# Performance work log

Measured on AMD Instinct MI355X. Metric: run time of the kernel, lower is better.

Reference implementation:

```python
import jax, jax.numpy as jnp
import numpy as np

D_K = 766  # feature dim, also softmax temperature per module init
NEG = -1000000000.0


def setup_inputs() -> dict:
    key = jax.random.key(0)
    k1, k2, k3 = jax.random.split(key, 3)
    B, H, L, D = 2, 4, 2048, D_K
    Q = jax.random.normal(k1, (B, H, L, D), dtype=jnp.float32)
    K = jax.random.normal(k2, (B, H, L, D), dtype=jnp.float32)
    attn_mask = jax.random.randint(k3, (B, H, L, L), 0, 2) > 0  # bool [B,H,Lk,Lq]
    return {"Q": Q, "K": K, "attn_mask": attn_mask}


def reference(Q, K, attn_mask):
    # scores: [B,H,Lq,Lk]
    scores = jnp.einsum("bhqd,bhkd->bhqk", Q, K) / np.sqrt(D_K).astype(np.float32)
    # mask is [B,H,Lk,Lq]; torch applies mask.transpose(2,3)
    scores = jnp.where(jnp.swapaxes(attn_mask, 2, 3), NEG, scores)
    attn1 = jax.nn.softmax(scores, axis=-1)                       # row softmax
    attn2 = jax.nn.softmax(jnp.swapaxes(scores, -1, -2), axis=-1)  # col softmax
    # dropout prob = 0.0 -> identity
    context1 = jnp.einsum("bhqk,bhkd->bhqd", attn1, K)
    context2 = jnp.einsum("bhkq,bhqd->bhkd", attn2, Q)
    return (context1, context2, attn1, attn2)
```

## Files before the change

### kernel.cpp

```cpp
#include <hip/hip_runtime.h>
#include <math.h>

#define L 2048
#define DK 766
#define DKP 768
#define NBH 8
#define NR (NBH * L)
#define NEGV -1000000000.0f

typedef __attribute__((ext_vector_type(8))) short bf16x8_t;
typedef __attribute__((ext_vector_type(4))) float f32x4_t;

#define LDT 72

typedef __attribute__((address_space(1))) const unsigned int gu32;
typedef __attribute__((address_space(3))) unsigned int lu32;

__device__ __forceinline__ short f2bf(float x) {
    union { float f; unsigned u; } v;
    v.f = x;
    unsigned r = v.u + 0x7fff + ((v.u >> 16) & 1);
    return (short)(r >> 16);
}

__device__ __forceinline__ float bf2f(short s) {
    union { unsigned u; float f; } v;
    v.u = ((unsigned)(unsigned short)s) << 16;
    return v.f;
}

__device__ __forceinline__ void gl_lds16(const void* g, void* l) {
    __builtin_amdgcn_global_load_lds((gu32*)g, (lu32*)l, 16, 0, 0);
}

#define BARR() asm volatile("s_barrier" ::: "memory")
#define VMW() asm volatile("s_waitcnt vmcnt(0)" ::: "memory")
#define PRIO1() __builtin_amdgcn_s_setprio(1)
#define PRIO0() __builtin_amdgcn_s_setprio(0)

__global__ __launch_bounds__(256) void k_cvtT(const float* __restrict__ Q,
                                              const float* __restrict__ K,
                                              short* __restrict__ Qb,
                                              short* __restrict__ Kb,
                                              short* __restrict__ Qt,
                                              short* __restrict__ Kt) {
    __shared__ short T[64 * LDT];
    const int tz = blockIdx.z;
    const int bh = tz & 7;
    const float* X = (tz < 8) ? Q : K;
    short* Xb = (tz < 8) ? Qb : Kb;
    short* Xt = (tz < 8) ? Qt : Kt;
    X += (size_t)bh * L * DK;
    Xb += (size_t)bh * L * DKP;
    Xt += (size_t)bh * DKP * L;
    const int r0 = blockIdx.y * 64, c0 = blockIdx.x * 64;
    const int t = threadIdx.x;
    const int rl = t >> 2, cc = (t & 3) * 16;

    bf16x8_t v0, v1;
#pragma unroll
    for (int p = 0; p < 8; ++p) {
        int c = c0 + cc + 2 * p;
        float2 f = (c < DK) ? *(const float2*)&X[(size_t)(r0 + rl) * DK + c]
                            : make_float2(0.f, 0.f);
        if (p < 4) { v0[2 * p] = f2bf(f.x); v0[2 * p + 1] = f2bf(f.y); }
        else { v1[2 * (p - 4)] = f2bf(f.x); v1[2 * (p - 4) + 1] = f2bf(f.y); }
    }
    *(bf16x8_t*)&Xb[(size_t)(r0 + rl) * DKP + c0 + cc] = v0;
    *(bf16x8_t*)&Xb[(size_t)(r0 + rl) * DKP + c0 + cc + 8] = v1;
    *(bf16x8_t*)&T[rl * LDT + cc] = v0;
    *(bf16x8_t*)&T[rl * LDT + cc + 8] = v1;
    __syncthreads();
    bf16x8_t w0, w1;
#pragma unroll
    for (int p = 0; p < 8; ++p) {
        w0[p] = T[(cc + p) * LDT + rl];
        w1[p] = T[(cc + 8 + p) * LDT + rl];
    }
    *(bf16x8_t*)&Xt[(size_t)(c0 + rl) * L + r0 + cc] = w0;
    *(bf16x8_t*)&Xt[(size_t)(c0 + rl) * L + r0 + cc + 8] = w1;
}

__global__ __launch_bounds__(512, 2) void k_score8(const short* __restrict__ Kb,
                                                   const short* __restrict__ Qb,
                                                   const int* __restrict__ mask,
                                                   short* __restrict__ Sb,
                                                   float* __restrict__ prowM,
                                                   float* __restrict__ prowS,
                                                   float* __restrict__ pcolM,
                                                   float* __restrict__ pcolS) {
    __shared__ __align__(16) short LB[65536];

    int flat = blockIdx.x;
    int nw = (flat & 7) * 64 + (flat >> 3);
    int bh = nw >> 6, rem = nw & 63;
    int byp = rem >> 3, bxp = rem & 7;
    const short* Am = Kb + (size_t)bh * L * DKP;
    const short* Bm = Qb + (size_t)bh * L * DKP;
    const int* Mm = mask + (size_t)bh * L * L;
    short* Sm = Sb + (size_t)bh * L * L;
    const int m0 = byp * 256, n0 = bxp * 256;

    const int t = threadIdx.x, lane = t & 63, wid = t >> 6;
    const int wr = wid >> 2, wc = wid & 3;
    const int lr = lane & 15, lg = lane >> 4;

    const int schunk = (lane & 7) ^ (lane >> 3);
    const short* aSrc = Am + (size_t)(m0 + wid * 8 + (lane >> 3)) * DKP + schunk * 8;
    const short* bSrc = Bm + (size_t)(n0 + wid * 8 + (lane >> 3)) * DKP + schunk * 8;
    char* ldsA = (char*)LB;
    char* ldsB = (char*)LB + 65536;

#define STAGEA(cb, k0n)                                                                 \
    do {                                                                                \
        gl_lds16(aSrc + (k0n), ldsA + (cb)*32768 + wid * 1024);                         \
        gl_lds16(aSrc + (size_t)64 * DKP + (k0n), ldsA + (cb)*32768 + 8192 + wid * 1024);  \
        gl_lds16(aSrc + (size_t)128 * DKP + (k0n), ldsA + (cb)*32768 + 16384 + wid * 1024); \
        gl_lds16(aSrc + (size_t)192 * DKP + (k0n), ldsA + (cb)*32768 + 24576 + wid * 1024); \
    } while (0)
#define STAGEB(cb, k0n)                                                                 \
    do {                                                                                \
        gl_lds16(bSrc + (k0n), ldsB + (cb)*32768 + wid * 1024);                         \
        gl_lds16(bSrc + (size_t)64 * DKP + (k0n), ldsB + (cb)*32768 + 8192 + wid * 1024);  \
        gl_lds16(bSrc + (size_t)128 * DKP + (k0n), ldsB + (cb)*32768 + 16384 + wid * 1024); \
        gl_lds16(bSrc + (size_t)192 * DKP + (k0n), ldsB + (cb)*32768 + 24576 + wid * 1024); \
    } while (0)

    const int axr = lr & 7;
    const int kc0 = ((0 + lg) ^ axr) * 8;
    const int kc1 = ((4 + lg) ^ axr) * 8;
    const int aRd = wr * 8192 + lr * 64;
    const int bRd = 32768 + (wc >> 1) * 8192 + ((wc & 1) * 64 + lr) * 64;

#define LDA0(c, i) (*(const bf16x8_t*)&LB[(c)*16384 + aRd + (i)*1024 + kc0])
#define LDA1(c, i) (*(const bf16x8_t*)&LB[(c)*16384 + aRd + (i)*1024 + kc1])
#define LDB0(c, j) (*(const bf16x8_t*)&LB[(c)*16384 + bRd + (j)*1024 + kc0])
#define LDB1(c, j) (*(const bf16x8_t*)&LB[(c)*16384 + bRd + (j)*1024 + kc1])

    f32x4_t acc[8][4];
#pragma unroll
    for (int i = 0; i < 8; ++i)
#pragma unroll
        for (int j = 0; j < 4; ++j) acc[i][j] = f32x4_t{0.f, 0.f, 0.f, 0.f};

    bf16x8_t bfr[4][2];

#define PHASE(c, i0, EXTRA)                                                             \
    do {                                                                                \
        bf16x8_t a00 = LDA0(c, i0), a01 = LDA1(c, i0);                                  \
        bf16x8_t a10 = LDA0(c, (i0) + 1), a11 = LDA1(c, (i0) + 1);                      \
        EXTRA;                                                                          \
        BARR();                                                                         \
        PRIO1();                                                                        \
        _Pragma("unroll") for (int j = 0; j < 4; ++j) {                                 \
            acc[i0][j] = __builtin_amdgcn_mfma_f32_16x16x32_bf16(a00, bfr[j][0],        \
                                                                 acc[i0][j], 0, 0, 0);  \
            acc[i0][j] = __builtin_amdgcn_mfma_f32_16x16x32_bf16(a01, bfr[j][1],        \
                                                                 acc[i0][j], 0, 0, 0);  \
            acc[(i0) + 1][j] = __builtin_amdgcn_mfma_f32_16x16x32_bf16(                 \
                a10, bfr[j][0], acc[(i0) + 1][j], 0, 0, 0);                             \
            acc[(i0) + 1][j] = __builtin_amdgcn_mfma_f32_16x16x32_bf16(                 \
                a11, bfr[j][1], acc[(i0) + 1][j], 0, 0, 0);                             \
        }                                                                               \
        PRIO0();                                                                        \
    } while (0)

    const int NT = DKP / 64;
    STAGEA(0, 0);
    STAGEB(0, 0);
    VMW();
    BARR();

    for (int kt = 0; kt < NT; ++kt) {
        const int c = kt & 1;
        const bool ds = (kt + 1 < NT);
        const int k0n = (kt + 1) * 64;
#pragma unroll
        for (int j = 0; j < 4; ++j) {
            bfr[j][0] = LDB0(c, j);
            bfr[j][1] = LDB1(c, j);
        }
        PHASE(c, 0, if (ds) STAGEA(c ^ 1, k0n));
        BARR();
        PHASE(c, 2, if (ds) STAGEB(c ^ 1, k0n));
        BARR();
        PHASE(c, 4, ((void)0));
        BARR();
        PHASE(c, 6, ((void)0));
        if (ds) VMW();
        BARR();
    }

    const float scale = 1.0f / sqrtf((float)DK);
#pragma unroll
    for (int i = 0; i < 8; ++i) {
        int krow = m0 + wr * 128 + i * 16 + lg * 4;
#pragma unroll
        for (int j = 0; j < 4; ++j) {
            int qcol = n0 + wc * 64 + j * 16 + lr;
#pragma unroll
            for (int r = 0; r < 4; ++r) {
                int mv = Mm[(size_t)(krow + r) * L + qcol];
                float v = mv ? NEGV : acc[i][j][r] * scale;
                acc[i][j][r] = v;
                Sm[(size_t)(krow + r) * L + qcol] = f2bf(v);
            }
        }
    }

    __syncthreads();
    float* redb = (float*)LB;

#pragma unroll
    for (int i = 0; i < 8; ++i) {
#pragma unroll
        for (int r = 0; r < 4; ++r) {
            float rm = fmaxf(fmaxf(acc[i][0][r], acc[i][1][r]),
                             fmaxf(acc[i][2][r], acc[i][3][r]));
#pragma unroll
            for (int m = 1; m < 16; m <<= 1) rm = fmaxf(rm, __shfl_xor(rm, m, 64));
            float rs = 0.f;
#pragma unroll
            for (int j = 0; j < 4; ++j) rs += expf(acc[i][j][r] - rm);
#pragma unroll
            for (int m = 1; m < 16; m <<= 1) rs += __shfl_xor(rs, m, 64);
            if (lr == 0) {
                int kr = wr * 128 + i * 16 + lg * 4 + r;
                redb[wc * 256 + kr] = rm;
                redb[1024 + wc * 256 + kr] = rs;
            }
        }
    }
#pragma unroll
    for (int j = 0; j < 4; ++j) {
        float cm = -INFINITY;
#pragma unroll
        for (int i = 0; i < 8; ++i)
#pragma unroll
            for (int r = 0; r < 4; ++r) cm = fmaxf(cm, acc[i][j][r]);
        cm = fmaxf(cm, __shfl_xor(cm, 16, 64));
        cm = fmaxf(cm, __shfl_xor(cm, 32, 64));
        float cs = 0.f;
#pragma unroll
        for (int i = 0; i < 8; ++i)
#pragma unroll
            for (int r = 0; r < 4; ++r) cs += expf(acc[i][j][r] - cm);
        cs += __shfl_xor(cs, 16, 64);
        cs += __shfl_xor(cs, 32, 64);
        if (lg == 0) {
            int qc = wc * 64 + j * 16 + lr;
            redb[2048 + wr * 256 + qc] = cm;
            redb[2560 + wr * 256 + qc] = cs;
        }
    }
    __syncthreads();
    if (t < 256) {
        float m = redb[t];
        float s = 0.f;
#pragma unroll
        for (int w = 1; w < 4; ++w) m = fmaxf(m, redb[w * 256 + t]);
#pragma unroll
        for (int w = 0; w < 4; ++w)
            s += redb[1024 + w * 256 + t] * expf(redb[w * 256 + t] - m);
        size_t o = (size_t)bxp * NR + bh * L + m0 + t;
        prowM[o] = m;
        prowS[o] = s;
    } else {
        int qc = t - 256;
        float mA = redb[2048 + qc], mB = redb[2048 + 256 + qc];
        float sA = redb[2560 + qc], sB = redb[2560 + 256 + qc];
        float m = fmaxf(mA, mB);
        float s = sA * expf(mA - m) + sB * expf(mB - m);
        size_t o = (size_t)byp * NR + bh * L + n0 + qc;
        pcolM[o] = m;
        pcolS[o] = s;
    }
#undef PHASE
#undef STAGEA
#undef STAGEB
#undef LDA0
#undef LDA1
#undef LDB0
#undef LDB1
}

__global__ __launch_bounds__(256) void k_comb8(const float* __restrict__ prowM,
                                               const float* __restrict__ prowS,
                                               const float* __restrict__ pcolM,
                                               const float* __restrict__ pcolS,
                                               float* __restrict__ m1,
                                               float* __restrict__ r1,
                                               float* __restrict__ m2,
                                               float* __restrict__ r2) {
    int idx = blockIdx.x * 256 + threadIdx.x;
    float m = -INFINITY;
#pragma unroll
    for (int c = 0; c < 8; ++c) m = fmaxf(m, prowM[(size_t)c * NR + idx]);
    float s = 0.f;
#pragma unroll
    for (int c = 0; c < 8; ++c)
        s += prowS[(size_t)c * NR + idx] * expf(prowM[(size_t)c * NR + idx] - m);
    m2[idx] = m;
    r2[idx] = 1.0f / s;

    m = -INFINITY;
#pragma unroll
    for (int c = 0; c < 8; ++c) m = fmaxf(m, pcolM[(size_t)c * NR + idx]);
    s = 0.f;
#pragma unroll
    for (int c = 0; c < 8; ++c)
        s += pcolS[(size_t)c * NR + idx] * expf(pcolM[(size_t)c * NR + idx] - m);
    m1[idx] = m;
    r1[idx] = 1.0f / s;
}

__global__ __launch_bounds__(256) void k_apply(const short* __restrict__ Sb,
                                               const float* __restrict__ mr,
                                               const float* __restrict__ rr,
                                               const float* __restrict__ mc,
                                               const float* __restrict__ rc,
                                               float* __restrict__ OutIn,
                                               float* __restrict__ OutTr,
                                               short* __restrict__ bIn,
                                               short* __restrict__ bTr) {
    __shared__ float T[64][65];
    const int bh = blockIdx.z;
    const int rb0 = blockIdx.x * 64, cb0 = blockIdx.y * 64;
    const short* Sm = Sb + (size_t)bh * L * L;
    float* Oin = OutIn + (size_t)bh * L * L;
    float* Otr = OutTr + (size_t)bh * L * L;
    const int t = threadIdx.x, tx = t & 15, ty = t >> 4;

    float4 mcv = *(const float4*)&mc[bh * L + cb0 + tx * 4];
    float4 rcv = *(const float4*)&rc[bh * L + cb0 + tx * 4];

#pragma unroll
    for (int i = 0; i < 4; ++i) {
        int r = rb0 + ty * 4 + i;
        float mrv = mr[bh * L + r], rrv = rr[bh * L + r];
        short4 sx = *(const short4*)&Sm[(size_t)r * L + cb0 + tx * 4];
        float x0 = bf2f(sx.x), x1 = bf2f(sx.y), x2 = bf2f(sx.z), x3 = bf2f(sx.w);
        float4 e = make_float4(expf(x0 - mrv) * rrv, expf(x1 - mrv) * rrv,
                               expf(x2 - mrv) * rrv, expf(x3 - mrv) * rrv);
        *(float4*)&Oin[(size_t)r * L + cb0 + tx * 4] = e;
        short4 b = make_short4(f2bf(e.x), f2bf(e.y), f2bf(e.z), f2bf(e.w));
        *(short4*)&bIn[(size_t)bh * L * L + (size_t)r * L + cb0 + tx * 4] = b;
        T[tx * 4 + 0][ty * 4 + i] = expf(x0 - mcv.x) * rcv.x;
        T[tx * 4 + 1][ty * 4 + i] = expf(x1 - mcv.y) * rcv.y;
        T[tx * 4 + 2][ty * 4 + i] = expf(x2 - mcv.z) * rcv.z;
        T[tx * 4 + 3][ty * 4 + i] = expf(x3 - mcv.w) * rcv.w;
    }
    __syncthreads();
#pragma unroll
    for (int i = 0; i < 4; ++i) {
        int c = ty * 4 + i;
        float4 v = make_float4(T[c][tx * 4], T[c][tx * 4 + 1], T[c][tx * 4 + 2],
                               T[c][tx * 4 + 3]);
        *(float4*)&Otr[(size_t)(cb0 + c) * L + rb0 + tx * 4] = v;
        short4 b = make_short4(f2bf(v.x), f2bf(v.y), f2bf(v.z), f2bf(v.w));
        *(short4*)&bTr[(size_t)bh * L * L + (size_t)(cb0 + c) * L + rb0 + tx * 4] = b;
    }
}

__global__ __launch_bounds__(512, 2) void k_ctx8(const short* __restrict__ a1b,
                                                 const short* __restrict__ a2b,
                                                 const short* __restrict__ Kt,
                                                 const short* __restrict__ Qt,
                                                 float* __restrict__ c1,
                                                 float* __restrict__ c2) {
    __shared__ __align__(16) short LB[57344];

    int flat = blockIdx.x;
    int nw = (flat & 7) * 64 + (flat >> 3);
    int inst = nw >> 5, rem = nw & 31;
    int myp = rem >> 2, nxp = rem & 3;
    int bh = inst & 7;
    const short* Am = ((inst < 8) ? a1b : a2b) + (size_t)bh * L * L;
    const short* Bt = ((inst < 8) ? Kt : Qt) + (size_t)bh * DKP * L;
    float* Cm = ((inst < 8) ? c1 : c2) + (size_t)bh * L * DK;
    const int m0 = myp * 256, n0 = nxp * 192;

    const int t = threadIdx.x, lane = t & 63, wid = t >> 6;
    const int wr = wid >> 2, wc = wid & 3;
    const int lr = lane & 15, lg = lane >> 4;

    const int schunk = (lane & 7) ^ (lane >> 3);
    const short* aSrc = Am + (size_t)(m0 + wid * 8 + (lane >> 3)) * L + schunk * 8;
    const short* bSrc = Bt + (size_t)(n0 + wid * 8 + (lane >> 3)) * L + schunk * 8;
    char* ldsA = (char*)LB;
    char* ldsB = (char*)LB + 65536;

#define STAGEA(cb, k0n)                                                               \
    do {                                                                              \
        gl_lds16(aSrc + (k0n), ldsA + (cb)*32768 + wid * 1024);                       \
        gl_lds16(aSrc + (size_t)64 * L + (k0n), ldsA + (cb)*32768 + 8192 + wid * 1024); \
        gl_lds16(aSrc + (size_t)128 * L + (k0n), ldsA + (cb)*32768 + 16384 + wid * 1024); \
        gl_lds16(aSrc + (size_t)192 * L + (k0n), ldsA + (cb)*32768 + 24576 + wid * 1024); \
    } while (0)
#define STAGEB(cb, k0n)                                                               \
    do {                                                                              \
        gl_lds16(bSrc + (k0n), ldsB + (cb)*24576 + wid * 1024);                       \
        gl_lds16(bSrc + (size_t)64 * L + (k0n), ldsB + (cb)*24576 + 8192 + wid * 1024); \
        gl_lds16(bSrc + (size_t)128 * L + (k0n), ldsB + (cb)*24576 + 16384 + wid * 1024); \
    } while (0)

    const int axr = lr & 7;
    const int kc0 = ((0 + lg) ^ axr) * 8;
    const int kc1 = ((4 + lg) ^ axr) * 8;
    const int aRd = wr * 8192 + lr * 64;
    const int bRd = 32768 + (wc * 48 + lr) * 64;

#define LDA0(c, i) (*(const bf16x8_t*)&LB[(c)*16384 + aRd + (i)*1024 + kc0])
#define LDA1(c, i) (*(const bf16x8_t*)&LB[(c)*16384 + aRd + (i)*1024 + kc1])
#define LDB0(c, j) (*(const bf16x8_t*)&LB[bRd + (c)*12288 + (j)*1024 + kc0])
#define LDB1(c, j) (*(const bf16x8_t*)&LB[bRd + (c)*12288 + (j)*1024 + kc1])

    f32x4_t acc[8][3];
#pragma unroll
    for (int i = 0; i < 8; ++i)
#pragma unroll
        for (int j = 0; j < 3; ++j) acc[i][j] = f32x4_t{0.f, 0.f, 0.f, 0.f};

    bf16x8_t bfr[3][2];

#define PHASE(c, i0, EXTRA)                                                           \
    do {                                                                              \
        bf16x8_t a00 = LDA0(c, i0), a01 = LDA1(c, i0);                                \
        bf16x8_t a10 = LDA0(c, (i0) + 1), a11 = LDA1(c, (i0) + 1);                    \
        EXTRA;                                                                        \
        BARR();                                                                       \
        PRIO1();                                                                      \
        _Pragma("unroll") for (int j = 0; j < 3; ++j) {                               \
            acc[i0][j] = __builtin_amdgcn_mfma_f32_16x16x32_bf16(a00, bfr[j][0],      \
                                                                 acc[i0][j], 0, 0, 0); \
            acc[i0][j] = __builtin_amdgcn_mfma_f32_16x16x32_bf16(a01, bfr[j][1],      \
                                                                 acc[i0][j], 0, 0, 0); \
            acc[(i0) + 1][j] = __builtin_amdgcn_mfma_f32_16x16x32_bf16(               \
                a10, bfr[j][0], acc[(i0) + 1][j], 0, 0, 0);                           \
            acc[(i0) + 1][j] = __builtin_amdgcn_mfma_f32_16x16x32_bf16(               \
                a11, bfr[j][1], acc[(i0) + 1][j], 0, 0, 0);                           \
        }                                                                             \
        PRIO0();                                                                      \
    } while (0)

    const int NT = L / 64;
    STAGEA(0, 0);
    STAGEB(0, 0);
    VMW();
    BARR();

    for (int kt = 0; kt < NT; ++kt) {
        const int c = kt & 1;
        const bool ds = (kt + 1 < NT);
        const int k0n = (kt + 1) * 64;
#pragma unroll
        for (int j = 0; j < 3; ++j) {
            bfr[j][0] = LDB0(c, j);
            bfr[j][1] = LDB1(c, j);
        }
        PHASE(c, 0, if (ds) STAGEA(c ^ 1, k0n));
        BARR();
        PHASE(c, 2, if (ds) STAGEB(c ^ 1, k0n));
        BARR();
        PHASE(c, 4, ((void)0));
        BARR();
        PHASE(c, 6, ((void)0));
        if (ds) VMW();
        BARR();
    }

#pragma unroll
    for (int i = 0; i < 8; ++i) {
        int row = m0 + wr * 128 + i * 16 + lg * 4;
#pragma unroll
        for (int j = 0; j < 3; ++j) {
            int col = n0 + wc * 48 + j * 16 + lr;
            if (col < DK) {
#pragma unroll
                for (int r = 0; r < 4; ++r)
                    Cm[(size_t)(row + r) * DK + col] = acc[i][j][r];
            }
        }
    }
#undef PHASE
#undef STAGEA
#undef STAGEB
#undef LDA0
#undef LDA1
#undef LDB0
#undef LDB1
}

extern "C" void kernel_launch(void* const* d_in, const int* in_sizes, int n_in,
                              void* d_out, int out_size, void* d_ws, size_t ws_size,
                              hipStream_t stream) {
    const float* Q = (const float*)d_in[0];
    const float* K = (const float*)d_in[1];
    const int* mask = (const int*)d_in[2];
    float* out = (float*)d_out;

    const size_t CTX = (size_t)NBH * L * DK;
    const size_t ATT = (size_t)NBH * L * L;
    float* c1 = out;
    float* c2 = out + CTX;
    float* a1 = out + 2 * CTX;
    float* a2 = out + 2 * CTX + ATT;

    float* ws = (float*)d_ws;
    float* m1 = ws;
    float* r1 = ws + NR;
    float* m2 = ws + 2 * (size_t)NR;
    float* r2 = ws + 3 * (size_t)NR;
    const size_t QBE = (size_t)NBH * L * DKP;
    short* Qb = (short*)(ws + 4 * (size_t)NR);
    short* Kb = Qb + QBE;
    short* a1b = Kb + QBE;
    short* a2b = a1b + ATT;
    short* Qt = a2b + ATT;
    short* Kt = Qt + QBE;

    float* prowM = c1;
    float* prowS = c1 + 8 * (size_t)NR;
    float* pcolM = c1 + 16 * (size_t)NR;
    float* pcolS = c1 + 24 * (size_t)NR;

    dim3 blk(256);

    k_cvtT<<<dim3(12, 32, 16), blk, 0, stream>>>(Q, K, Qb, Kb, Qt, Kt);
    k_score8<<<dim3(512), dim3(512), 0, stream>>>(Kb, Qb, mask, a2b, prowM, prowS,
                                                  pcolM, pcolS);
    k_comb8<<<dim3(NR / 256), blk, 0, stream>>>(prowM, prowS, pcolM, pcolS, m1, r1,
                                                m2, r2);
    k_apply<<<dim3(32, 32, NBH), blk, 0, stream>>>(a2b, m2, r2, m1, r1, a2, a1, a2b,
                                                   a1b);
    k_ctx8<<<dim3(512), dim3(512), 0, stream>>>(a1b, a2b, Kt, Qt, c1, c2);
}
```

Baseline: 431.8 us.

## Make score blocks compute two adjacent output tiles with prefetch across tiles

Each k_score8 workgroup now processes two 256x256 score tiles sharing the same K rows, halving the grid to 256 blocks. The first k-chunk of the second tile's operands is prefetched during the last k-step of the first tile, so the epilogue (mask, store, softmax partials) of tile one overlaps with loads for tile two. The reduction buffer moves to a different LDS region to avoid clobbering the prefetched data. This cuts per-block startup and pipeline-fill cost, but gives fewer blocks than CUs (256 on a 256-CU part at 2 blocks/CU occupancy), which may leave some parallelism unused.

```diff
diff --git a/kernel.cpp b/kernel.cpp
--- a/kernel.cpp
+++ b/kernel.cpp
@@ -92,14 +92,14 @@
     __shared__ __align__(16) short LB[65536];
 
     int flat = blockIdx.x;
-    int nw = (flat & 7) * 64 + (flat >> 3);
-    int bh = nw >> 6, rem = nw & 63;
-    int byp = rem >> 3, bxp = rem & 7;
+    int nw = (flat & 7) * 32 + (flat >> 3);
+    int bh = nw >> 5, rem = nw & 31;
+    int byp = rem >> 2, bxq = rem & 3;
     const short* Am = Kb + (size_t)bh * L * DKP;
     const short* Bm = Qb + (size_t)bh * L * DKP;
     const int* Mm = mask + (size_t)bh * L * L;
     short* Sm = Sb + (size_t)bh * L * L;
-    const int m0 = byp * 256, n0 = bxp * 256;
+    const int m0 = byp * 256;
 
     const int t = threadIdx.x, lane = t & 63, wid = t >> 6;
     const int wr = wid >> 2, wc = wid & 3;
@@ -107,23 +107,24 @@
 
     const int schunk = (lane & 7) ^ (lane >> 3);
     const short* aSrc = Am + (size_t)(m0 + wid * 8 + (lane >> 3)) * DKP + schunk * 8;
-    const short* bSrc = Bm + (size_t)(n0 + wid * 8 + (lane >> 3)) * DKP + schunk * 8;
+    const short* bSrc0 =
+        Bm + (size_t)(bxq * 512 + wid * 8 + (lane >> 3)) * DKP + schunk * 8;
     char* ldsA = (char*)LB;
     char* ldsB = (char*)LB + 65536;
 
-#define STAGEA(cb, k0n)                                                                 \
+#define STAGEAp(P, cb, k0n)                                                             \
     do {                                                                                \
-        gl_lds16(aSrc + (k0n), ldsA + (cb)*32768 + wid * 1024);                         \
-        gl_lds16(aSrc + (size_t)64 * DKP + (k0n), ldsA + (cb)*32768 + 8192 + wid * 1024);  \
-        gl_lds16(aSrc + (size_t)128 * DKP + (k0n), ldsA + (cb)*32768 + 16384 + wid * 1024); \
-        gl_lds16(aSrc + (size_t)192 * DKP + (k0n), ldsA + (cb)*32768 + 24576 + wid * 1024); \
+        gl_lds16((P) + (k0n), ldsA + (cb)*32768 + wid * 1024);                          \
+        gl_lds16((P) + (size_t)64 * DKP + (k0n), ldsA + (cb)*32768 + 8192 + wid * 1024);   \
+        gl_lds16((P) + (size_t)128 * DKP + (k0n), ldsA + (cb)*32768 + 16384 + wid * 1024); \
+        gl_lds16((P) + (size_t)192 * DKP + (k0n), ldsA + (cb)*32768 + 24576 + wid * 1024); \
     } while (0)
-#define STAGEB(cb, k0n)                                                                 \
+#define STAGEBp(P, cb, k0n)                                                             \
     do {                                                                                \
-        gl_lds16(bSrc + (k0n), ldsB + (cb)*32768 + wid * 1024);                         \
-        gl_lds16(bSrc + (size_t)64 * DKP + (k0n), ldsB + (cb)*32768 + 8192 + wid * 1024);  \
-        gl_lds16(bSrc + (size_t)128 * DKP + (k0n), ldsB + (cb)*32768 + 16384 + wid * 1024); \
-        gl_lds16(bSrc + (size_t)192 * DKP + (k0n), ldsB + (cb)*32768 + 24576 + wid * 1024); \
+        gl_lds16((P) + (k0n), ldsB + (cb)*32768 + wid * 1024);                          \
+        gl_lds16((P) + (size_t)64 * DKP + (k0n), ldsB + (cb)*32768 + 8192 + wid * 1024);   \
+        gl_lds16((P) + (size_t)128 * DKP + (k0n), ldsB + (cb)*32768 + 16384 + wid * 1024); \
+        gl_lds16((P) + (size_t)192 * DKP + (k0n), ldsB + (cb)*32768 + 24576 + wid * 1024); \
     } while (0)
 
     const int axr = lr & 7;
@@ -138,11 +139,6 @@
 #define LDB1(c, j) (*(const bf16x8_t*)&LB[(c)*16384 + bRd + (j)*1024 + kc1])
 
     f32x4_t acc[8][4];
-#pragma unroll
-    for (int i = 0; i < 8; ++i)
-#pragma unroll
-        for (int j = 0; j < 4; ++j) acc[i][j] = f32x4_t{0.f, 0.f, 0.f, 0.f};
-
     bf16x8_t bfr[4][2];
 
 #define PHASE(c, i0, EXTRA)                                                             \
@@ -166,118 +162,148 @@
     } while (0)
 
     const int NT = DKP / 64;
-    STAGEA(0, 0);
-    STAGEB(0, 0);
-    VMW();
-    BARR();
-
-    for (int kt = 0; kt < NT; ++kt) {
-        const int c = kt & 1;
-        const bool ds = (kt + 1 < NT);
-        const int k0n = (kt + 1) * 64;
+
+    for (int pp = 0; pp < 2; ++pp) {
+        const int bxp = bxq * 2 + pp;
+        const int n0 = bxp * 256;
+        const short* bSrc = bSrc0 + (size_t)pp * 256 * DKP;
+        const short* bSrcN = bSrc0 + (size_t)256 * DKP;
+
+#pragma unroll
+        for (int i = 0; i < 8; ++i)
+#pragma unroll
+            for (int j = 0; j < 4; ++j) acc[i][j] = f32x4_t{0.f, 0.f, 0.f, 0.f};
+
+        if (pp == 0) {
+            STAGEAp(aSrc, 0, 0);
+            STAGEBp(bSrc, 0, 0);
+        }
+        VMW();
+        BARR();
+
+        for (int kt = 0; kt < NT - 1; ++kt) {
+            const int c = kt & 1;
+            const int k0n = (kt + 1) * 64;
+#pragma unroll
+            for (int j = 0; j < 4; ++j) {
+                bfr[j][0] = LDB0(c, j);
+                bfr[j][1] = LDB1(c, j);
+            }
+            PHASE(c, 0, STAGEAp(aSrc, c ^ 1, k0n));
+            BARR();
+            PHASE(c, 2, STAGEBp(bSrc, c ^ 1, k0n));
+            BARR();
+            PHASE(c, 4, ((void)0));
+            BARR();
+            PHASE(c, 6, ((void)0));
+            VMW();
+            BARR();
+        }
+        {
+            const int c = 1;
+#pragma unroll
+            for (int j = 0; j < 4; ++j) {
+                bfr[j][0] = LDB0(c, j);
+                bfr[j][1] = LDB1(c, j);
+            }
+            PHASE(c, 0, if (pp == 0) STAGEAp(aSrc, 0, 0));
+            BARR();
+            PHASE(c, 2, if (pp == 0) STAGEBp(bSrcN, 0, 0));
+            BARR();
+            PHASE(c, 4, ((void)0));
+            BARR();
+            PHASE(c, 6, ((void)0));
+            BARR();
+        }
+
+        const float scale = 1.0f / sqrtf((float)DK);
+#pragma unroll
+        for (int i = 0; i < 8; ++i) {
+            int krow = m0 + wr * 128 + i * 16 + lg * 4;
+#pragma unroll
+            for (int j = 0; j < 4; ++j) {
+                int qcol = n0 + wc * 64 + j * 16 + lr;
+#pragma unroll
+                for (int r = 0; r < 4; ++r) {
+                    int mv = Mm[(size_t)(krow + r) * L + qcol];
+                    float v = mv ? NEGV : acc[i][j][r] * scale;
+                    acc[i][j][r] = v;
+                    Sm[(size_t)(krow + r) * L + qcol] = f2bf(v);
+                }
+            }
+        }
+
+        __syncthreads();
+        float* redb = (float*)&LB[16384];
+
+#pragma unroll
+        for (int i = 0; i < 8; ++i) {
+#pragma unroll
+            for (int r = 0; r < 4; ++r) {
+                float rm = fmaxf(fmaxf(acc[i][0][r], acc[i][1][r]),
+                                 fmaxf(acc[i][2][r], acc[i][3][r]));
+#pragma unroll
+                for (int m = 1; m < 16; m <<= 1) rm = fmaxf(rm, __shfl_xor(rm, m, 64));
+                float rs = 0.f;
+#pragma unroll
+                for (int j = 0; j < 4; ++j) rs += expf(acc[i][j][r] - rm);
+#pragma unroll
+                for (int m = 1; m < 16; m <<= 1) rs += __shfl_xor(rs, m, 64);
+                if (lr == 0) {
+                    int kr = wr * 128 + i * 16 + lg * 4 + r;
+                    redb[wc * 256 + kr] = rm;
+                    redb[1024 + wc * 256 + kr] = rs;
+                }
+            }
+        }
 #pragma unroll
         for (int j = 0; j < 4; ++j) {
-            bfr[j][0] = LDB0(c, j);
-            bfr[j][1] = LDB1(c, j);
-        }
-        PHASE(c, 0, if (ds) STAGEA(c ^ 1, k0n));
-        BARR();
-        PHASE(c, 2, if (ds) STAGEB(c ^ 1, k0n));
-        BARR();
-        PHASE(c, 4, ((void)0));
-        BARR();
-        PHASE(c, 6, ((void)0));
-        if (ds) VMW();
-        BARR();
-    }
-
-    const float scale = 1.0f / sqrtf((float)DK);
-#pragma unroll
-    for (int i = 0; i < 8; ++i) {
-        int krow = m0 + wr * 128 + i * 16 + lg * 4;
-#pragma unroll
-        for (int j = 0; j < 4; ++j) {
-            int qcol = n0 + wc * 64 + j * 16 + lr;
-#pragma unroll
-            for (int r = 0; r < 4; ++r) {
-                int mv = Mm[(size_t)(krow + r) * L + qcol];
-                float v = mv ? NEGV : acc[i][j][r] * scale;
-                acc[i][j][r] = v;
-                Sm[(size_t)(krow + r) * L + qcol] = f2bf(v);
+            float cm = -INFINITY;
+#pragma unroll
+            for (int i = 0; i < 8; ++i)
+#pragma unroll
+                for (int r = 0; r < 4; ++r) cm = fmaxf(cm, acc[i][j][r]);
+            cm = fmaxf(cm, __shfl_xor(cm, 16, 64));
+            cm = fmaxf(cm, __shfl_xor(cm, 32, 64));
+            float cs = 0.f;
+#pragma unroll
+            for (int i = 0; i < 8; ++i)
+#pragma unroll
+                for (int r = 0; r < 4; ++r) cs += expf(acc[i][j][r] - cm);
+            cs += __shfl_xor(cs, 16, 64);
+            cs += __shfl_xor(cs, 32, 64);
+            if (lg == 0) {
+                int qc = wc * 64 + j * 16 + lr;
+                redb[2048 + wr * 256 + qc] = cm;
+                redb[2560 + wr * 256 + qc] = cs;
             }
         }
-    }
-
-    __syncthreads();
-    float* redb = (float*)LB;
-
-#pragma unroll
-    for (int i = 0; i < 8; ++i) {
-#pragma unroll
-        for (int r = 0; r < 4; ++r) {
-            float rm = fmaxf(fmaxf(acc[i][0][r], acc[i][1][r]),
-                             fmaxf(acc[i][2][r], acc[i][3][r]));
-#pragma unroll
-            for (int m = 1; m < 16; m <<= 1) rm = fmaxf(rm, __shfl_xor(rm, m, 64));
-            float rs = 0.f;
-#pragma unroll
-            for (int j = 0; j < 4; ++j) rs += expf(acc[i][j][r] - rm);
-#pragma unroll
-            for (int m = 1; m < 16; m <<= 1) rs += __shfl_xor(rs, m, 64);
-            if (lr == 0) {
-                int kr = wr * 128 + i * 16 + lg * 4 + r;
-                redb[wc * 256 + kr] = rm;
-                redb[1024 + wc * 256 + kr] = rs;
-            }
-        }
-    }
-#pragma unroll
-    for (int j = 0; j < 4; ++j) {
-        float cm = -INFINITY;
-#pragma unroll
-        for (int i = 0; i < 8; ++i)
-#pragma unroll
-            for (int r = 0; r < 4; ++r) cm = fmaxf(cm, acc[i][j][r]);
-        cm = fmaxf(cm, __shfl_xor(cm, 16, 64));
-        cm = fmaxf(cm, __shfl_xor(cm, 32, 64));
-        float cs = 0.f;
-#pragma unroll
-        for (int i = 0; i < 8; ++i)
-#pragma unroll
-            for (int r = 0; r < 4; ++r) cs += expf(acc[i][j][r] - cm);
-        cs += __shfl_xor(cs, 16, 64);
-        cs += __shfl_xor(cs, 32, 64);
-        if (lg == 0) {
-            int qc = wc * 64 + j * 16 + lr;
-            redb[2048 + wr * 256 + qc] = cm;
-            redb[2560 + wr * 256 + qc] = cs;
-        }
-    }
-    __syncthreads();
-    if (t < 256) {
-        float m = redb[t];
-        float s = 0.f;
-#pragma unroll
-        for (int w = 1; w < 4; ++w) m = fmaxf(m, redb[w * 256 + t]);
-#pragma unroll
-        for (int w = 0; w < 4; ++w)
-            s += redb[1024 + w * 256 + t] * expf(redb[w * 256 + t] - m);
-        size_t o = (size_t)bxp * NR + bh * L + m0 + t;
-        prowM[o] = m;
-        prowS[o] = s;
-    } else {
-        int qc = t - 256;
-        float mA = redb[2048 + qc], mB = redb[2048 + 256 + qc];
-        float sA = redb[2560 + qc], sB = redb[2560 + 256 + qc];
-        float m = fmaxf(mA, mB);
-        float s = sA * expf(mA - m) + sB * expf(mB - m);
-        size_t o = (size_t)byp * NR + bh * L + n0 + qc;
-        pcolM[o] = m;
-        pcolS[o] = s;
+        __syncthreads();
+        if (t < 256) {
+            float m = redb[t];
+            float s = 0.f;
+#pragma unroll
+            for (int w = 1; w < 4; ++w) m = fmaxf(m, redb[w * 256 + t]);
+#pragma unroll
+            for (int w = 0; w < 4; ++w)
+                s += redb[1024 + w * 256 + t] * expf(redb[w * 256 + t] - m);
+            size_t o = (size_t)bxp * NR + bh * L + m0 + t;
+            prowM[o] = m;
+            prowS[o] = s;
+        } else {
+            int qc = t - 256;
+            float mA = redb[2048 + qc], mB = redb[2048 + 256 + qc];
+            float sA = redb[2560 + qc], sB = redb[2560 + 256 + qc];
+            float m = fmaxf(mA, mB);
+            float s = sA * expf(mA - m) + sB * expf(mB - m);
+            size_t o = (size_t)byp * NR + bh * L + n0 + qc;
+            pcolM[o] = m;
+            pcolS[o] = s;
+        }
     }
 #undef PHASE
-#undef STAGEA
-#undef STAGEB
+#undef STAGEAp
+#undef STAGEBp
 #undef LDA0
 #undef LDA1
 #undef LDB0
@@ -527,7 +553,7 @@
     dim3 blk(256);
 
     k_cvtT<<<dim3(12, 32, 16), blk, 0, stream>>>(Q, K, Qb, Kb, Qt, Kt);
-    k_score8<<<dim3(512), dim3(512), 0, stream>>>(Kb, Qb, mask, a2b, prowM, prowS,
+    k_score8<<<dim3(256), dim3(512), 0, stream>>>(Kb, Qb, mask, a2b, prowM, prowS,
                                                   pcolM, pcolS);
     k_comb8<<<dim3(NR / 256), blk, 0, stream>>>(prowM, prowS, pcolM, pcolS, m1, r1,
                                                 m2, r2);
```

After: 523.5 us. 21.2% more time.
